# Optimization experiments

Measured on AMD Instinct MI355X. Metric: run time of the kernel, lower is better.

## Reference

```python
import jax, jax.numpy as jnp
from jax import lax
import numpy as np

B, CIN, H, S = 32, 16, 64, 128
TAU = 0.5


def _conv1d(x, w, b, dilation):
    # x: [B, C, S], w: [O, I, K] -> [B, O, S], stride 1, SAME padding (matches torch padding='same')
    y = lax.conv_general_dilated(x, w, window_strides=(1,), padding='SAME',
                                 rhs_dilation=(dilation,),
                                 dimension_numbers=('NCH', 'OIH', 'NCH'))
    return y + b[None, :, None]


def setup_inputs() -> dict:
    key = jax.random.key(0)
    ks = jax.random.split(key, 16)
    def w(k, shape, fan_in):
        return jax.random.normal(k, shape, jnp.float32) * (1.0 / np.sqrt(fan_in))
    inp = {
        'data': jax.random.normal(ks[0], (B, 1, CIN, S), jnp.float32),
        'conv11_w': w(ks[1], (H, CIN, 1), CIN), 'conv11_b': jnp.zeros((H,), jnp.float32),
        'conv12_w': w(ks[2], (H, H, 3), H * 3), 'conv12_b': jnp.zeros((H,), jnp.float32),
        'conv21_w': w(ks[3], (H, CIN, 1), CIN), 'conv21_b': jnp.zeros((H,), jnp.float32),
        'conv22_w': w(ks[4], (H, H, 5), H * 5), 'conv22_b': jnp.zeros((H,), jnp.float32),
        'conv31_w': w(ks[5], (H, CIN, 5), CIN * 5), 'conv31_b': jnp.zeros((H,), jnp.float32),
        'fc_final_w': w(ks[6], (H, 3 * H), 3 * H), 'fc_final_b': jnp.zeros((H,), jnp.float32),
        'fc1_w': w(ks[7], (H, 2 * H), 2 * H), 'fc1_b': jnp.zeros((H,), jnp.float32),
        'fc2_w': w(ks[8], (2, H), H), 'fc2_b': jnp.zeros((2,), jnp.float32),
        # pre-sampled uniform noise for gumbel-softmax (deterministic reference)
        'gumbel_u': jax.random.uniform(ks[9], (B, S * S, 2), jnp.float32, 1e-7, 1.0 - 1e-7),
    }
    return inp


def reference(data, conv11_w, conv11_b, conv12_w, conv12_b, conv21_w, conv21_b,
              conv22_w, conv22_b, conv31_w, conv31_b, fc_final_w, fc_final_b,
              fc1_w, fc1_b, fc2_w, fc2_b, gumbel_u):
    x = data[:, 0].astype(jnp.float32)                      # [B, CIN, S]
    x1 = _conv1d(_conv1d(x, conv11_w, conv11_b, 1), conv12_w, conv12_b, 3)
    x2 = _conv1d(_conv1d(x, conv21_w, conv21_b, 1), conv22_w, conv22_b, 5)
    x3 = _conv1d(x, conv31_w, conv31_b, 1)
    h = jnp.concatenate([x1, x2, x3], axis=1)               # [B, 3H, S]
    h = jnp.swapaxes(h, 1, 2)                               # [B, S, 3H]
    h = jax.nn.relu(h @ fc_final_w.T + fc_final_b)          # [B, S, H]

    # one-hot matmuls are exact gathers: rec rows = repeat, send cols = tile
    rows = jnp.repeat(jnp.arange(S), S)                     # [S*S]
    cols = jnp.tile(jnp.arange(S), S)                       # [S*S]
    receivers = h[:, rows]                                  # [B, S*S, H]
    senders = h[:, cols]                                    # [B, S*S, H]
    e = jnp.concatenate([senders, receivers], axis=2)       # [B, S*S, 2H]
    e = jax.nn.relu(e @ fc1_w.T + fc1_b)
    logits = e @ fc2_w.T + fc2_b                            # [B, S*S, 2]

    # gumbel-softmax, hard=True (straight-through)
    g = -jnp.log(-jnp.log(gumbel_u))
    y_soft = jax.nn.softmax((logits + g) / TAU, axis=-1)
    y_hard = jax.nn.one_hot(jnp.argmax(y_soft, axis=-1), 2, dtype=y_soft.dtype)
    y = lax.stop_gradient(y_hard - y_soft) + y_soft

    a = y[..., 0].reshape(-1, S, S)                         # [B, S, S]
    keep = jnp.triu(jnp.ones((S, S), bool), k=1)            # zero lower tri and diagonal
    return jnp.where(keep, a, jnp.zeros((), a.dtype))
```

## Files before the change

### kernel.cpp

```cpp
#include <hip/hip_runtime.h>
#include <math.h>

#define BB   32
#define CIN  16
#define HH   64
#define SS   128

typedef double f64x4 __attribute__((ext_vector_type(4)));
#define MFMA64(a,b,c) __builtin_amdgcn_mfma_f64_16x16x4f64((a),(b),(c),0,0,0)

__global__ __launch_bounds__(256) void prep_weights(
    const float* __restrict__ w11, const float* __restrict__ w21,
    const float* __restrict__ w12, const float* __restrict__ w22,
    const float* __restrict__ w31, const float* __restrict__ wf,
    const float* __restrict__ w1,  float* __restrict__ W)
{
    int i = blockIdx.x * 256 + threadIdx.x;
    if (i < 1024)       { int k=i>>4, c=i&15;                  W[c*64+k]          = w11[i]; }
    else if (i < 2048)  { int j=i-1024;  int k=j>>4, c=j&15;   W[1024 + c*64+k]   = w21[j]; }
    else if (i < 14336) { int j=i-2048;  int n=j/192, r=j-192*n; W[2048 + r*64+n] = w12[j]; }
    else if (i < 34816) { int j=i-14336; int n=j/320, r=j-320*n; W[14336 + r*64+n]= w22[j]; }
    else if (i < 43008) { int j=i-34816; int r=j>>6, n=j&63;   W[34816 + j] = (r<80)? w31[n*80+r] : 0.f; }
    else if (i < 55296) { int j=i-43008; int n=j/192, r=j-192*n; W[43008 + r*64+n]= wf[j]; }
    else if (i < 59392) { int j=i-55296; int n=j>>6, m=j&63;   W[55296 + m*64+n]  = w1[n*128+m]; }
    else if (i < 63488) { int j=i-59392; int n=j>>6, m=j&63;   W[59392 + m*64+n]  = w1[n*128+64+m]; }
}

__device__ __forceinline__ void loadB(float* dst, const float* __restrict__ Bb, int c) {
    const float* s = Bb + c * 4096;
    #pragma unroll
    for (int q = 0; q < 16; ++q) dst[q] = s[q * 256];
}
__device__ __forceinline__ void mfma_chunk(const double* pA, const float* cb,
                                           f64x4& a0, f64x4& a1, f64x4& a2, f64x4& a3) {
    #pragma unroll
    for (int s = 0; s < 16; s += 4) {
        a0 = MFMA64(pA[(s+0)*64], (double)cb[s+0], a0);
        a1 = MFMA64(pA[(s+1)*64], (double)cb[s+1], a1);
        a2 = MFMA64(pA[(s+2)*64], (double)cb[s+2], a2);
        a3 = MFMA64(pA[(s+3)*64], (double)cb[s+3], a3);
    }
}

__global__ __launch_bounds__(256, 1) void fused_front(
    const float* __restrict__ x,
    const float* __restrict__ b11, const float* __restrict__ b12,
    const float* __restrict__ b21, const float* __restrict__ b22,
    const float* __restrict__ b31, const float* __restrict__ bf,
    const float* __restrict__ b1,  const float* __restrict__ Wsrc,
    double* __restrict__ Qg, double* __restrict__ Pg)
{
    const int b  = blockIdx.y;
    const int s0 = blockIdx.x * 16;
    const int t  = threadIdx.x;
    const int lane = t & 63, wave = t >> 6;

    __shared__ float  xl[CIN][37];
    __shared__ float  wA[2048];
    __shared__ double t1e[48 * 64];
    __shared__ double t2e[80 * 64];
    __shared__ double x3e[32 * 64];
    __shared__ double x123[16][196];
    double* he = x3e;

    int rowi[4], colj[4], mA1, mA2, bn, bkk;
    {
        double lv = (double)lane;
        f64x4 zz{0.0, 0.0, 0.0, 0.0};
        f64x4 d1 = MFMA64(lv, 1.0, zz);
        f64x4 d2 = MFMA64(1.0, lv, zz);
        int am = ((((int)d1[0]) & 3) == 0);
        int bm = ((((int)d2[0]) & 3) == 0);
        for (int r = 0; r < 4; ++r) {
            int v1 = (int)d1[r], v2 = (int)d2[r];
            rowi[r] = (am ? (v1 - 96) >> 2 : (v1 - 6) >> 4) & 15;
            colj[r] = (bm ? (v2 - 96) >> 2 : (v2 - 6) >> 4) & 15;
        }
        mA1 = am ? 16 : 1;  mA2 = am ? 1 : 4;
        bn  = bm ? (lane & 15) : (lane >> 2);
        bkk = bm ? (lane >> 4) : (lane & 3);
    }
    const float* Bb = Wsrc + 2048 + bkk * 64 + (wave << 4) + bn;

    float bufa[16], bufb[16];
    loadB(bufa, Bb, 0);

    for (int e = t; e < 2048; e += 256) wA[e] = Wsrc[e];
    for (int e = t; e < CIN * 36; e += 256) {
        int c = e / 36, col = e - c * 36;
        int g = s0 - 10 + col;
        xl[c][col] = (g >= 0 && g < SS) ? x[(b * CIN + c) * SS + g] : 0.f;
    }
    __syncthreads();

    for (int e = t; e < 1408; e += 256) {
        int k = e & 63, col = e >> 6;
        int g = s0 - 3 + col;
        double val = 0.0;
        if (g >= 0 && g < SS) {
            double u0 = (double)b11[k], u1 = 0.0;
            #pragma unroll
            for (int c = 0; c < CIN; c += 2) {
                u0 += (double)xl[c][col + 7]     * (double)wA[c * 64 + k];
                u1 += (double)xl[c + 1][col + 7] * (double)wA[(c + 1) * 64 + k];
            }
            val = u0 + u1;
        }
        #pragma unroll
        for (int tp = 0; tp < 3; ++tp) {
            int p = col - 3 * tp;
            if (p >= 0 && p < 16) {
                int kk = k * 3 + tp;
                t1e[((kk>>2)<<6) + (kk&3)*mA1 + p*mA2] = val;
            }
        }
    }
    for (int e = t; e < 2304; e += 256) {
        int k = e & 63, col = e >> 6;
        int g = s0 - 10 + col;
        double val = 0.0;
        if (g >= 0 && g < SS) {
            double u0 = (double)b21[k], u1 = 0.0;
            #pragma unroll
            for (int c = 0; c < CIN; c += 2) {
                u0 += (double)xl[c][col]     * (double)wA[1024 + c * 64 + k];
                u1 += (double)xl[c + 1][col] * (double)wA[1024 + (c + 1) * 64 + k];
            }
            val = u0 + u1;
        }
        #pragma unroll
        for (int tp = 0; tp < 5; ++tp) {
            int p = col - 5 * tp;
            if (p >= 0 && p < 16) {
                int kk = k * 5 + tp;
                t2e[((kk>>2)<<6) + (kk&3)*mA1 + p*mA2] = val;
            }
        }
    }
    for (int e = t; e < 2048; e += 256) {
        int p = e & 15, kk = e >> 4;
        double val = 0.0;
        if (kk < 80) { int c = kk / 5, tp = kk - c * 5; val = (double)xl[c][p + 8 + tp]; }
        x3e[((kk>>2)<<6) + (kk&3)*mA1 + p*mA2] = val;
    }
    __syncthreads();

    {
        f64x4 a0{0,0,0,0}, a1{0,0,0,0}, a2{0,0,0,0}, a3{0,0,0,0};
        loadB(bufb, Bb, 1);  mfma_chunk(t1e + lane,        bufa, a0,a1,a2,a3);
        loadB(bufa, Bb, 2);  mfma_chunk(t1e + 1024 + lane, bufb, a0,a1,a2,a3);
        loadB(bufb, Bb, 3);  mfma_chunk(t1e + 2048 + lane, bufa, a0,a1,a2,a3);
        f64x4 acm = (a0 + a1) + (a2 + a3);
        for (int r = 0; r < 4; ++r) {
            int ch = (wave << 4) + colj[r];
            x123[rowi[r]][ch] = acm[r] + (double)b12[ch];
        }
    }
    {
        f64x4 a0{0,0,0,0}, a1{0,0,0,0}, a2{0,0,0,0}, a3{0,0,0,0};
        loadB(bufa, Bb, 4);  mfma_chunk(t2e + lane,        bufb, a0,a1,a2,a3);
        loadB(bufb, Bb, 5);  mfma_chunk(t2e + 1024 + lane, bufa, a0,a1,a2,a3);
        loadB(bufa, Bb, 6);  mfma_chunk(t2e + 2048 + lane, bufb, a0,a1,a2,a3);
        loadB(bufb, Bb, 7);  mfma_chunk(t2e + 3072 + lane, bufa, a0,a1,a2,a3);
        loadB(bufa, Bb, 8);  mfma_chunk(t2e + 4096 + lane, bufb, a0,a1,a2,a3);
        f64x4 acm = (a0 + a1) + (a2 + a3);
        for (int r = 0; r < 4; ++r) {
            int ch = (wave << 4) + colj[r];
            x123[rowi[r]][64 + ch] = acm[r] + (double)b22[ch];
        }
    }
    {
        f64x4 a0{0,0,0,0}, a1{0,0,0,0}, a2{0,0,0,0}, a3{0,0,0,0};
        loadB(bufb, Bb, 9);  mfma_chunk(x3e + lane,        bufa, a0,a1,a2,a3);
        loadB(bufa, Bb, 10); mfma_chunk(x3e + 1024 + lane, bufb, a0,a1,a2,a3);
        f64x4 acm = (a0 + a1) + (a2 + a3);
        for (int r = 0; r < 4; ++r) {
            int ch = (wave << 4) + colj[r];
            x123[rowi[r]][128 + ch] = acm[r] + (double)b31[ch];
        }
    }
    __syncthreads();
    for (int e = t; e < 3072; e += 256) {
        int p = e & 15, k = e >> 4;
        t1e[((k>>2)<<6) + (k&3)*mA1 + p*mA2] = x123[p][k];
    }
    __syncthreads();
    {
        f64x4 a0{0,0,0,0}, a1{0,0,0,0}, a2{0,0,0,0}, a3{0,0,0,0};
        loadB(bufb, Bb, 11); mfma_chunk(t1e + lane,        bufa, a0,a1,a2,a3);
        loadB(bufa, Bb, 12); mfma_chunk(t1e + 1024 + lane, bufb, a0,a1,a2,a3);
        loadB(bufb, Bb, 13); mfma_chunk(t1e + 2048 + lane, bufa, a0,a1,a2,a3);
        f64x4 acm = (a0 + a1) + (a2 + a3);
        for (int r = 0; r < 4; ++r) {
            int m = (wave << 4) + colj[r];
            double v = acm[r] + (double)bf[m];
            he[((m>>2)<<6) + (m&3)*mA1 + rowi[r]*mA2] = v > 0.0 ? v : 0.0;
        }
    }
    __syncthreads();
    {
        f64x4 a0{0,0,0,0}, a1{0,0,0,0}, a2{0,0,0,0}, a3{0,0,0,0};
        loadB(bufa, Bb, 14); mfma_chunk(he + lane, bufb, a0,a1,a2,a3);
        f64x4 acm = (a0 + a1) + (a2 + a3);
        for (int r = 0; r < 4; ++r)
            Qg[((long)b * SS + s0 + rowi[r]) * HH + (wave << 4) + colj[r]] = acm[r];
    }
    {
        f64x4 a0{0,0,0,0}, a1{0,0,0,0}, a2{0,0,0,0}, a3{0,0,0,0};
        mfma_chunk(he + lane, bufa, a0,a1,a2,a3);
        f64x4 acm = (a0 + a1) + (a2 + a3);
        for (int r = 0; r < 4; ++r) {
            int ch = (wave << 4) + colj[r];
            Pg[((long)b * SS + s0 + rowi[r]) * HH + ch] = acm[r] + (double)b1[ch];
        }
    }
}

__global__ __launch_bounds__(256) void edges(
    const double* __restrict__ Qg, const double* __restrict__ Pg,
    const float* __restrict__ w2, const float* __restrict__ b2,
    const float* __restrict__ gum, float* __restrict__ out)
{
    const int b   = blockIdx.y;
    const int tit = blockIdx.x >> 3;
    const int tjt = blockIdx.x & 7;
    const int t   = threadIdx.x;
    const int ti  = t >> 4, tj = t & 15;
    const int i   = tit * 16 + ti;
    const int j   = tjt * 16 + tj;
    float* op = out + ((long)b * SS + i) * SS + j;

    if (tjt < tit) { *op = 0.0f; return; }

    __shared__ float Plf[16][68];
    __shared__ float Qlf[16][68];
    __shared__ float dwl[64];

    if (t < 64) dwl[t] = w2[t] - w2[64 + t];
    for (int idx = t; idx < 1024; idx += 256) {
        int r = idx >> 6, c = idx & 63;
        Plf[r][c] = (float)Pg[((long)b * SS + tit * 16 + r) * HH + c];
        Qlf[r][c] = (float)Qg[((long)b * SS + tjt * 16 + r) * HH + c];
    }
    __syncthreads();

    if (j <= i) { *op = 0.0f; return; }

    long e = (long)b * SS * SS + (long)i * SS + j;
    const float2 uv = *(const float2*)(gum + e * 2);
    float basef = (b2[0] - b2[1]) - logf(-logf(uv.x)) + logf(-logf(uv.y));

    const float2* Pr = (const float2*)(&Plf[ti][0]);
    const float2* Qr = (const float2*)(&Qlf[tj][0]);
    const float2* Dr = (const float2*)dwl;
    float s0 = 0.f, s1 = 0.f;
    #pragma unroll
    for (int k2 = 0; k2 < 32; ++k2) {
        float2 pv = Pr[k2], qv = Qr[k2], dv = Dr[k2];
        float v0 = pv.x + qv.x; v0 = v0 > 0.f ? v0 : 0.f;
        float v1 = pv.y + qv.y; v1 = v1 > 0.f ? v1 : 0.f;
        s0 += v0 * dv.x; s1 += v1 * dv.y;
    }
    float tot = basef + s0 + s1;

    if (fabsf(tot) < 3e-3f) {
        const double* Prd = Pg + ((long)b * SS + i) * HH;
        const double* Qrd = Qg + ((long)b * SS + j) * HH;
        double acc = (double)b2[0] - (double)b2[1]
                   - log(-log((double)uv.x)) + log(-log((double)uv.y));
        for (int k = 0; k < 64; ++k) {
            double v = Prd[k] + Qrd[k];
            if (v > 0.0) acc += v * ((double)w2[k] - (double)w2[64 + k]);
        }
        *op = (acc >= 0.0) ? 1.0f : 0.0f;
    } else {
        *op = (tot >= 0.f) ? 1.0f : 0.0f;
    }
}

extern "C" void kernel_launch(void* const* d_in, const int* in_sizes, int n_in,
                              void* d_out, int out_size, void* d_ws, size_t ws_size,
                              hipStream_t stream) {
    const float* data = (const float*)d_in[0];
    const float* w11  = (const float*)d_in[1];
    const float* b11  = (const float*)d_in[2];
    const float* w12  = (const float*)d_in[3];
    const float* b12  = (const float*)d_in[4];
    const float* w21  = (const float*)d_in[5];
    const float* b21  = (const float*)d_in[6];
    const float* w22  = (const float*)d_in[7];
    const float* b22  = (const float*)d_in[8];
    const float* w31  = (const float*)d_in[9];
    const float* b31  = (const float*)d_in[10];
    const float* wf   = (const float*)d_in[11];
    const float* bf   = (const float*)d_in[12];
    const float* w1   = (const float*)d_in[13];
    const float* b1   = (const float*)d_in[14];
    const float* w2   = (const float*)d_in[15];
    const float* b2   = (const float*)d_in[16];
    const float* gum  = (const float*)d_in[17];
    float* out = (float*)d_out;

    double* Qg = (double*)d_ws;
    double* Pg = Qg + (long)BB * SS * HH;
    float*  Wt = (float*)(Pg + (long)BB * SS * HH);

    prep_weights<<<248, 256, 0, stream>>>(w11, w21, w12, w22, w31, wf, w1, Wt);
    fused_front<<<dim3(8, BB), 256, 0, stream>>>(
        data, b11, b12, b21, b22, b31, bf, b1, Wt, Qg, Pg);
    edges<<<dim3(64, BB), 256, 0, stream>>>(Qg, Pg, w2, b2, gum, out);
}
```

Baseline: 51.39 us.

## Split K across two wave groups in fused_front with LDS reduction

Doubles the fused_front workgroup to 512 threads and splits each MFMA chunk's K range between two halves of waves. Partial accumulators go through a shared buffer and are summed by the lower half before bias and store. This targets the serial MFMA latency chain of the front kernel when each CU holds only one block. It adds extra barriers and LDS traffic per stage.

```diff
diff --git a/kernel.cpp b/kernel.cpp
--- a/kernel.cpp
+++ b/kernel.cpp
@@ -26,23 +26,34 @@
     else if (i < 63488) { int j=i-59392; int n=j>>6, m=j&63;   W[59392 + m*64+n]  = w1[n*128+64+m]; }
 }
 
-__device__ __forceinline__ void loadB(float* dst, const float* __restrict__ Bb, int c) {
-    const float* s = Bb + c * 4096;
+__device__ __forceinline__ void loadB8(float* dst, const float* __restrict__ Bb,
+                                       int c, int koff) {
+    const float* s = Bb + c * 4096 + koff * 256;
     #pragma unroll
-    for (int q = 0; q < 16; ++q) dst[q] = s[q * 256];
-}
-__device__ __forceinline__ void mfma_chunk(const double* pA, const float* cb,
-                                           f64x4& a0, f64x4& a1, f64x4& a2, f64x4& a3) {
+    for (int q = 0; q < 8; ++q) dst[q] = s[q * 256];
+}
+__device__ __forceinline__ void loadB2(float* dst, const float* __restrict__ Bb,
+                                       int c, int koff) {
+    const float* s = Bb + c * 4096 + koff * 256;
+    dst[0] = s[0]; dst[1] = s[256];
+}
+__device__ __forceinline__ void mfma8(const double* pA, const float* cb, int boff,
+                                      f64x4& a0, f64x4& a1, f64x4& a2, f64x4& a3) {
     #pragma unroll
-    for (int s = 0; s < 16; s += 4) {
-        a0 = MFMA64(pA[(s+0)*64], (double)cb[s+0], a0);
-        a1 = MFMA64(pA[(s+1)*64], (double)cb[s+1], a1);
-        a2 = MFMA64(pA[(s+2)*64], (double)cb[s+2], a2);
-        a3 = MFMA64(pA[(s+3)*64], (double)cb[s+3], a3);
-    }
-}
-
-__global__ __launch_bounds__(256, 1) void fused_front(
+    for (int s = 0; s < 8; s += 4) {
+        a0 = MFMA64(pA[(boff+s+0)*64], (double)cb[s+0], a0);
+        a1 = MFMA64(pA[(boff+s+1)*64], (double)cb[s+1], a1);
+        a2 = MFMA64(pA[(boff+s+2)*64], (double)cb[s+2], a2);
+        a3 = MFMA64(pA[(boff+s+3)*64], (double)cb[s+3], a3);
+    }
+}
+__device__ __forceinline__ void mfma2(const double* pA, const float* cb, int boff,
+                                      f64x4& a0, f64x4& a1) {
+    a0 = MFMA64(pA[(boff+0)*64], (double)cb[0], a0);
+    a1 = MFMA64(pA[(boff+1)*64], (double)cb[1], a1);
+}
+
+__global__ __launch_bounds__(512, 1) void fused_front(
     const float* __restrict__ x,
     const float* __restrict__ b11, const float* __restrict__ b12,
     const float* __restrict__ b21, const float* __restrict__ b22,
@@ -54,6 +65,9 @@
     const int s0 = blockIdx.x * 16;
     const int t  = threadIdx.x;
     const int lane = t & 63, wave = t >> 6;
+    const int wv = wave & 3;
+    const int kh = wave >> 2;
+    const int kh8 = kh << 3, kh2 = kh << 1;
 
     __shared__ float  xl[CIN][37];
     __shared__ float  wA[2048];
@@ -61,6 +75,7 @@
     __shared__ double t2e[80 * 64];
     __shared__ double x3e[32 * 64];
     __shared__ double x123[16][196];
+    __shared__ double part[4][4][64];
     double* he = x3e;
 
     int rowi[4], colj[4], mA1, mA2, bn, bkk;
@@ -80,20 +95,20 @@
         bn  = bm ? (lane & 15) : (lane >> 2);
         bkk = bm ? (lane >> 4) : (lane & 3);
     }
-    const float* Bb = Wsrc + 2048 + bkk * 64 + (wave << 4) + bn;
-
-    float bufa[16], bufb[16];
-    loadB(bufa, Bb, 0);
-
-    for (int e = t; e < 2048; e += 256) wA[e] = Wsrc[e];
-    for (int e = t; e < CIN * 36; e += 256) {
+    const float* Bb = Wsrc + 2048 + bkk * 64 + (wv << 4) + bn;
+
+    float bufa[8], bufb[8];
+    loadB8(bufa, Bb, 0, kh8);
+
+    for (int e = t; e < 2048; e += 512) wA[e] = Wsrc[e];
+    for (int e = t; e < CIN * 36; e += 512) {
         int c = e / 36, col = e - c * 36;
         int g = s0 - 10 + col;
         xl[c][col] = (g >= 0 && g < SS) ? x[(b * CIN + c) * SS + g] : 0.f;
     }
     __syncthreads();
 
-    for (int e = t; e < 1408; e += 256) {
+    for (int e = t; e < 1408; e += 512) {
         int k = e & 63, col = e >> 6;
         int g = s0 - 3 + col;
         double val = 0.0;
@@ -115,7 +130,7 @@
             }
         }
     }
-    for (int e = t; e < 2304; e += 256) {
+    for (int e = t; e < 2304; e += 512) {
         int k = e & 63, col = e >> 6;
         int g = s0 - 10 + col;
         double val = 0.0;
@@ -137,7 +152,7 @@
             }
         }
     }
-    for (int e = t; e < 2048; e += 256) {
+    for (int e = t; e < 2048; e += 512) {
         int p = e & 15, kk = e >> 4;
         double val = 0.0;
         if (kk < 80) { int c = kk / 5, tp = kk - c * 5; val = (double)xl[c][p + 8 + tp]; }
@@ -147,71 +162,100 @@
 
     {
         f64x4 a0{0,0,0,0}, a1{0,0,0,0}, a2{0,0,0,0}, a3{0,0,0,0};
-        loadB(bufb, Bb, 1);  mfma_chunk(t1e + lane,        bufa, a0,a1,a2,a3);
-        loadB(bufa, Bb, 2);  mfma_chunk(t1e + 1024 + lane, bufb, a0,a1,a2,a3);
-        loadB(bufb, Bb, 3);  mfma_chunk(t1e + 2048 + lane, bufa, a0,a1,a2,a3);
-        f64x4 acm = (a0 + a1) + (a2 + a3);
-        for (int r = 0; r < 4; ++r) {
-            int ch = (wave << 4) + colj[r];
-            x123[rowi[r]][ch] = acm[r] + (double)b12[ch];
-        }
-    }
-    {
-        f64x4 a0{0,0,0,0}, a1{0,0,0,0}, a2{0,0,0,0}, a3{0,0,0,0};
-        loadB(bufa, Bb, 4);  mfma_chunk(t2e + lane,        bufb, a0,a1,a2,a3);
-        loadB(bufb, Bb, 5);  mfma_chunk(t2e + 1024 + lane, bufa, a0,a1,a2,a3);
-        loadB(bufa, Bb, 6);  mfma_chunk(t2e + 2048 + lane, bufb, a0,a1,a2,a3);
-        loadB(bufb, Bb, 7);  mfma_chunk(t2e + 3072 + lane, bufa, a0,a1,a2,a3);
-        loadB(bufa, Bb, 8);  mfma_chunk(t2e + 4096 + lane, bufb, a0,a1,a2,a3);
-        f64x4 acm = (a0 + a1) + (a2 + a3);
-        for (int r = 0; r < 4; ++r) {
-            int ch = (wave << 4) + colj[r];
-            x123[rowi[r]][64 + ch] = acm[r] + (double)b22[ch];
-        }
-    }
-    {
-        f64x4 a0{0,0,0,0}, a1{0,0,0,0}, a2{0,0,0,0}, a3{0,0,0,0};
-        loadB(bufb, Bb, 9);  mfma_chunk(x3e + lane,        bufa, a0,a1,a2,a3);
-        loadB(bufa, Bb, 10); mfma_chunk(x3e + 1024 + lane, bufb, a0,a1,a2,a3);
-        f64x4 acm = (a0 + a1) + (a2 + a3);
-        for (int r = 0; r < 4; ++r) {
-            int ch = (wave << 4) + colj[r];
-            x123[rowi[r]][128 + ch] = acm[r] + (double)b31[ch];
-        }
-    }
-    __syncthreads();
-    for (int e = t; e < 3072; e += 256) {
+        loadB8(bufb, Bb, 1, kh8);  mfma8(t1e + lane,        bufa, kh8, a0,a1,a2,a3);
+        loadB8(bufa, Bb, 2, kh8);  mfma8(t1e + 1024 + lane, bufb, kh8, a0,a1,a2,a3);
+        loadB8(bufb, Bb, 3, kh8);  mfma8(t1e + 2048 + lane, bufa, kh8, a0,a1,a2,a3);
+        f64x4 acm = (a0 + a1) + (a2 + a3);
+        if (kh) { for (int r = 0; r < 4; ++r) part[r][wv][lane] = acm[r]; }
+        __syncthreads();
+        if (!kh) {
+            for (int r = 0; r < 4; ++r) {
+                int ch = (wv << 4) + colj[r];
+                x123[rowi[r]][ch] = acm[r] + part[r][wv][lane] + (double)b12[ch];
+            }
+        }
+        __syncthreads();
+    }
+    {
+        f64x4 a0{0,0,0,0}, a1{0,0,0,0}, a2{0,0,0,0}, a3{0,0,0,0};
+        loadB8(bufa, Bb, 4, kh8);  mfma8(t2e + lane,        bufb, kh8, a0,a1,a2,a3);
+        loadB8(bufb, Bb, 5, kh8);  mfma8(t2e + 1024 + lane, bufa, kh8, a0,a1,a2,a3);
+        loadB8(bufa, Bb, 6, kh8);  mfma8(t2e + 2048 + lane, bufb, kh8, a0,a1,a2,a3);
+        loadB8(bufb, Bb, 7, kh8);  mfma8(t2e + 3072 + lane, bufa, kh8, a0,a1,a2,a3);
+        loadB8(bufa, Bb, 8, kh8);  mfma8(t2e + 4096 + lane, bufb, kh8, a0,a1,a2,a3);
+        f64x4 acm = (a0 + a1) + (a2 + a3);
+        if (kh) { for (int r = 0; r < 4; ++r) part[r][wv][lane] = acm[r]; }
+        __syncthreads();
+        if (!kh) {
+            for (int r = 0; r < 4; ++r) {
+                int ch = (wv << 4) + colj[r];
+                x123[rowi[r]][64 + ch] = acm[r] + part[r][wv][lane] + (double)b22[ch];
+            }
+        }
+        __syncthreads();
+    }
+    {
+        f64x4 a0{0,0,0,0}, a1{0,0,0,0}, a2{0,0,0,0}, a3{0,0,0,0};
+        loadB2(bufb, Bb, 9, kh2);  mfma8(x3e + lane,        bufa, kh8, a0,a1,a2,a3);
+        loadB8(bufa, Bb, 10, kh8); mfma2(x3e + 1024 + lane, bufb, kh2, a0,a1);
+        f64x4 acm = (a0 + a1) + (a2 + a3);
+        if (kh) { for (int r = 0; r < 4; ++r) part[r][wv][lane] = acm[r]; }
+        __syncthreads();
+        if (!kh) {
+            for (int r = 0; r < 4; ++r) {
+                int ch = (wv << 4) + colj[r];
+                x123[rowi[r]][128 + ch] = acm[r] + part[r][wv][lane] + (double)b31[ch];
+            }
+        }
+        __syncthreads();
+    }
+    for (int e = t; e < 3072; e += 512) {
         int p = e & 15, k = e >> 4;
         t1e[((k>>2)<<6) + (k&3)*mA1 + p*mA2] = x123[p][k];
     }
     __syncthreads();
     {
         f64x4 a0{0,0,0,0}, a1{0,0,0,0}, a2{0,0,0,0}, a3{0,0,0,0};
-        loadB(bufb, Bb, 11); mfma_chunk(t1e + lane,        bufa, a0,a1,a2,a3);
-        loadB(bufa, Bb, 12); mfma_chunk(t1e + 1024 + lane, bufb, a0,a1,a2,a3);
-        loadB(bufb, Bb, 13); mfma_chunk(t1e + 2048 + lane, bufa, a0,a1,a2,a3);
-        f64x4 acm = (a0 + a1) + (a2 + a3);
-        for (int r = 0; r < 4; ++r) {
-            int m = (wave << 4) + colj[r];
-            double v = acm[r] + (double)bf[m];
-            he[((m>>2)<<6) + (m&3)*mA1 + rowi[r]*mA2] = v > 0.0 ? v : 0.0;
-        }
-    }
-    __syncthreads();
-    {
-        f64x4 a0{0,0,0,0}, a1{0,0,0,0}, a2{0,0,0,0}, a3{0,0,0,0};
-        loadB(bufa, Bb, 14); mfma_chunk(he + lane, bufb, a0,a1,a2,a3);
-        f64x4 acm = (a0 + a1) + (a2 + a3);
-        for (int r = 0; r < 4; ++r)
-            Qg[((long)b * SS + s0 + rowi[r]) * HH + (wave << 4) + colj[r]] = acm[r];
-    }
-    {
-        f64x4 a0{0,0,0,0}, a1{0,0,0,0}, a2{0,0,0,0}, a3{0,0,0,0};
-        mfma_chunk(he + lane, bufa, a0,a1,a2,a3);
-        f64x4 acm = (a0 + a1) + (a2 + a3);
-        for (int r = 0; r < 4; ++r) {
-            int ch = (wave << 4) + colj[r];
-            Pg[((long)b * SS + s0 + rowi[r]) * HH + ch] = acm[r] + (double)b1[ch];
+        loadB8(bufb, Bb, 11, kh8); mfma8(t1e + lane,        bufa, kh8, a0,a1,a2,a3);
+        loadB8(bufa, Bb, 12, kh8); mfma8(t1e + 1024 + lane, bufb, kh8, a0,a1,a2,a3);
+        loadB8(bufb, Bb, 13, kh8); mfma8(t1e + 2048 + lane, bufa, kh8, a0,a1,a2,a3);
+        f64x4 acm = (a0 + a1) + (a2 + a3);
+        if (kh) { for (int r = 0; r < 4; ++r) part[r][wv][lane] = acm[r]; }
+        __syncthreads();
+        if (!kh) {
+            for (int r = 0; r < 4; ++r) {
+                int m = (wv << 4) + colj[r];
+                double v = acm[r] + part[r][wv][lane] + (double)bf[m];
+                he[((m>>2)<<6) + (m&3)*mA1 + rowi[r]*mA2] = v > 0.0 ? v : 0.0;
+            }
+        }
+        __syncthreads();
+    }
+    {
+        f64x4 a0{0,0,0,0}, a1{0,0,0,0}, a2{0,0,0,0}, a3{0,0,0,0};
+        loadB8(bufa, Bb, 14, kh8); mfma8(he + lane, bufb, kh8, a0,a1,a2,a3);
+        f64x4 acm = (a0 + a1) + (a2 + a3);
+        if (kh) { for (int r = 0; r < 4; ++r) part[r][wv][lane] = acm[r]; }
+        __syncthreads();
+        if (!kh) {
+            for (int r = 0; r < 4; ++r)
+                Qg[((long)b * SS + s0 + rowi[r]) * HH + (wv << 4) + colj[r]]
+                    = acm[r] + part[r][wv][lane];
+        }
+        __syncthreads();
+    }
+    {
+        f64x4 a0{0,0,0,0}, a1{0,0,0,0}, a2{0,0,0,0}, a3{0,0,0,0};
+        mfma8(he + lane, bufa, kh8, a0,a1,a2,a3);
+        f64x4 acm = (a0 + a1) + (a2 + a3);
+        if (kh) { for (int r = 0; r < 4; ++r) part[r][wv][lane] = acm[r]; }
+        __syncthreads();
+        if (!kh) {
+            for (int r = 0; r < 4; ++r) {
+                int ch = (wv << 4) + colj[r];
+                Pg[((long)b * SS + s0 + rowi[r]) * HH + ch]
+                    = acm[r] + part[r][wv][lane] + (double)b1[ch];
+            }
         }
     }
 }
@@ -306,7 +350,7 @@
     float*  Wt = (float*)(Pg + (long)BB * SS * HH);
 
     prep_weights<<<248, 256, 0, stream>>>(w11, w21, w12, w22, w31, wf, w1, Wt);
-    fused_front<<<dim3(8, BB), 256, 0, stream>>>(
+    fused_front<<<dim3(8, BB), 512, 0, stream>>>(
         data, b11, b12, b21, b22, b31, bf, b1, Wt, Qg, Pg);
     edges<<<dim3(64, BB), 256, 0, stream>>>(Qg, Pg, w2, b2, gum, out);
 }
```

Measured after the change: 49.21 us. 1.04x faster.

## Replace FP64 MFMA front-end with scalar FMA split-K and drop weight prep kernel

Applied to the files above, without the earlier changes.

Replaces the f64 MFMA-based conv/FC chain in the front kernel with per-lane scalar double FMAs. Each of 8 waves handles a slice of the reduction dimension, and a shared-memory reduction combines the partial sums. Weights are read directly from the original layouts, so the separate prep_weights launch and its transposed workspace copy go away. Block size doubles to 512 threads. This trades matrix-core throughput for fewer launches and simpler layouts, but adds several syncthreads-heavy reductions and strided global weight reads per lane.

```diff
diff --git a/kernel.cpp b/kernel.cpp
--- a/kernel.cpp
+++ b/kernel.cpp
@@ -6,48 +6,72 @@
 #define HH   64
 #define SS   128
 
-typedef double f64x4 __attribute__((ext_vector_type(4)));
-#define MFMA64(a,b,c) __builtin_amdgcn_mfma_f64_16x16x4f64((a),(b),(c),0,0,0)
-
-__global__ __launch_bounds__(256) void prep_weights(
-    const float* __restrict__ w11, const float* __restrict__ w21,
-    const float* __restrict__ w12, const float* __restrict__ w22,
-    const float* __restrict__ w31, const float* __restrict__ wf,
-    const float* __restrict__ w1,  float* __restrict__ W)
-{
-    int i = blockIdx.x * 256 + threadIdx.x;
-    if (i < 1024)       { int k=i>>4, c=i&15;                  W[c*64+k]          = w11[i]; }
-    else if (i < 2048)  { int j=i-1024;  int k=j>>4, c=j&15;   W[1024 + c*64+k]   = w21[j]; }
-    else if (i < 14336) { int j=i-2048;  int n=j/192, r=j-192*n; W[2048 + r*64+n] = w12[j]; }
-    else if (i < 34816) { int j=i-14336; int n=j/320, r=j-320*n; W[14336 + r*64+n]= w22[j]; }
-    else if (i < 43008) { int j=i-34816; int r=j>>6, n=j&63;   W[34816 + j] = (r<80)? w31[n*80+r] : 0.f; }
-    else if (i < 55296) { int j=i-43008; int n=j/192, r=j-192*n; W[43008 + r*64+n]= wf[j]; }
-    else if (i < 59392) { int j=i-55296; int n=j>>6, m=j&63;   W[55296 + m*64+n]  = w1[n*128+m]; }
-    else if (i < 63488) { int j=i-59392; int n=j>>6, m=j&63;   W[59392 + m*64+n]  = w1[n*128+64+m]; }
-}
-
-__device__ __forceinline__ void loadB(float* dst, const float* __restrict__ Bb, int c) {
-    const float* s = Bb + c * 4096;
+
+template <int KS>
+__device__ __forceinline__ void fma_slice(const double* __restrict__ dat,
+                                          const float* __restrict__ wrow,
+                                          double* acc) {
+    float wreg[KS];
     #pragma unroll
-    for (int q = 0; q < 16; ++q) dst[q] = s[q * 256];
-}
-__device__ __forceinline__ void mfma_chunk(const double* pA, const float* cb,
-                                           f64x4& a0, f64x4& a1, f64x4& a2, f64x4& a3) {
+    for (int q = 0; q < KS; q += 2)
+        *(float2*)(wreg + q) = *(const float2*)(wrow + q);
     #pragma unroll
-    for (int s = 0; s < 16; s += 4) {
-        a0 = MFMA64(pA[(s+0)*64], (double)cb[s+0], a0);
-        a1 = MFMA64(pA[(s+1)*64], (double)cb[s+1], a1);
-        a2 = MFMA64(pA[(s+2)*64], (double)cb[s+2], a2);
-        a3 = MFMA64(pA[(s+3)*64], (double)cb[s+3], a3);
-    }
-}
-
-__global__ __launch_bounds__(256, 1) void fused_front(
+    for (int p = 0; p < 16; ++p) acc[p] = 0.0;
+    #pragma unroll 4
+    for (int kk = 0; kk < KS; ++kk) {
+        const double2* dr = (const double2*)(dat + kk * 16);
+        double w = (double)wreg[kk];
+        #pragma unroll
+        for (int h2 = 0; h2 < 8; ++h2) {
+            double2 dv = dr[h2];
+            acc[2 * h2]     += dv.x * w;
+            acc[2 * h2 + 1] += dv.y * w;
+        }
+    }
+}
+
+__device__ __forceinline__ void reduce8(double* __restrict__ red,
+                                        const double* __restrict__ acc,
+                                        int wave, int lane, double* tot) {
+    __syncthreads();
+    if (wave >= 4) {
+        double* rp = red + (wave - 4) * 1024 + lane;
+        #pragma unroll
+        for (int p = 0; p < 16; ++p) rp[p * 64] = acc[p];
+    }
+    __syncthreads();
+    double acc2[16];
+    if (wave < 4) {
+        const double* rp = red + wave * 1024 + lane;
+        #pragma unroll
+        for (int p = 0; p < 16; ++p) acc2[p] = acc[p] + rp[p * 64];
+    }
+    __syncthreads();
+    if (wave < 4) {
+        double* rp = red + wave * 1024 + lane;
+        #pragma unroll
+        for (int p = 0; p < 16; ++p) rp[p * 64] = acc2[p];
+    }
+    __syncthreads();
+    if (wave < 4) {
+        #pragma unroll
+        for (int q = 0; q < 4; ++q) {
+            int p = 4 * wave + q;
+            tot[q] = red[p * 64 + lane]        + red[1024 + p * 64 + lane]
+                   + red[2048 + p * 64 + lane] + red[3072 + p * 64 + lane];
+        }
+    }
+}
+
+__global__ __launch_bounds__(512, 2) void fused_front(
     const float* __restrict__ x,
-    const float* __restrict__ b11, const float* __restrict__ b12,
-    const float* __restrict__ b21, const float* __restrict__ b22,
-    const float* __restrict__ b31, const float* __restrict__ bf,
-    const float* __restrict__ b1,  const float* __restrict__ Wsrc,
+    const float* __restrict__ w11, const float* __restrict__ b11,
+    const float* __restrict__ w12, const float* __restrict__ b12,
+    const float* __restrict__ w21, const float* __restrict__ b21,
+    const float* __restrict__ w22, const float* __restrict__ b22,
+    const float* __restrict__ w31, const float* __restrict__ b31,
+    const float* __restrict__ wf,  const float* __restrict__ bf,
+    const float* __restrict__ w1,  const float* __restrict__ b1,
     double* __restrict__ Qg, double* __restrict__ Pg)
 {
     const int b  = blockIdx.y;
@@ -55,45 +79,28 @@
     const int t  = threadIdx.x;
     const int lane = t & 63, wave = t >> 6;
 
+    __shared__ double S[14592];
     __shared__ float  xl[CIN][37];
     __shared__ float  wA[2048];
-    __shared__ double t1e[48 * 64];
-    __shared__ double t2e[80 * 64];
-    __shared__ double x3e[32 * 64];
-    __shared__ double x123[16][196];
-    double* he = x3e;
-
-    int rowi[4], colj[4], mA1, mA2, bn, bkk;
-    {
-        double lv = (double)lane;
-        f64x4 zz{0.0, 0.0, 0.0, 0.0};
-        f64x4 d1 = MFMA64(lv, 1.0, zz);
-        f64x4 d2 = MFMA64(1.0, lv, zz);
-        int am = ((((int)d1[0]) & 3) == 0);
-        int bm = ((((int)d2[0]) & 3) == 0);
-        for (int r = 0; r < 4; ++r) {
-            int v1 = (int)d1[r], v2 = (int)d2[r];
-            rowi[r] = (am ? (v1 - 96) >> 2 : (v1 - 6) >> 4) & 15;
-            colj[r] = (bm ? (v2 - 96) >> 2 : (v2 - 6) >> 4) & 15;
-        }
-        mA1 = am ? 16 : 1;  mA2 = am ? 1 : 4;
-        bn  = bm ? (lane & 15) : (lane >> 2);
-        bkk = bm ? (lane >> 4) : (lane & 3);
-    }
-    const float* Bb = Wsrc + 2048 + bkk * 64 + (wave << 4) + bn;
-
-    float bufa[16], bufb[16];
-    loadB(bufa, Bb, 0);
-
-    for (int e = t; e < 2048; e += 256) wA[e] = Wsrc[e];
-    for (int e = t; e < CIN * 36; e += 256) {
+    double* t2d = S;
+    double* x3d = S + 5120;
+    double* xf  = S + 6400;
+    double* h   = S + 9472;
+    double* t1d = S + 10496;
+    double* red = S + 10496;
+
+    for (int e = t; e < 2048; e += 512) {
+        if (e < 1024) { int k = e >> 4, c = e & 15; wA[c * 64 + k] = w11[e]; }
+        else { int j = e - 1024; int k = j >> 4, c = j & 15; wA[1024 + c * 64 + k] = w21[j]; }
+    }
+    for (int e = t; e < CIN * 36; e += 512) {
         int c = e / 36, col = e - c * 36;
         int g = s0 - 10 + col;
         xl[c][col] = (g >= 0 && g < SS) ? x[(b * CIN + c) * SS + g] : 0.f;
     }
     __syncthreads();
 
-    for (int e = t; e < 1408; e += 256) {
+    for (int e = t; e < 1408; e += 512) {
         int k = e & 63, col = e >> 6;
         int g = s0 - 3 + col;
         double val = 0.0;
@@ -109,13 +116,10 @@
         #pragma unroll
         for (int tp = 0; tp < 3; ++tp) {
             int p = col - 3 * tp;
-            if (p >= 0 && p < 16) {
-                int kk = k * 3 + tp;
-                t1e[((kk>>2)<<6) + (kk&3)*mA1 + p*mA2] = val;
-            }
-        }
-    }
-    for (int e = t; e < 2304; e += 256) {
+            if (p >= 0 && p < 16) t1d[(k * 3 + tp) * 16 + p] = val;
+        }
+    }
+    for (int e = t; e < 2304; e += 512) {
         int k = e & 63, col = e >> 6;
         int g = s0 - 10 + col;
         double val = 0.0;
@@ -131,87 +135,71 @@
         #pragma unroll
         for (int tp = 0; tp < 5; ++tp) {
             int p = col - 5 * tp;
-            if (p >= 0 && p < 16) {
-                int kk = k * 5 + tp;
-                t2e[((kk>>2)<<6) + (kk&3)*mA1 + p*mA2] = val;
-            }
-        }
-    }
-    for (int e = t; e < 2048; e += 256) {
-        int p = e & 15, kk = e >> 4;
-        double val = 0.0;
-        if (kk < 80) { int c = kk / 5, tp = kk - c * 5; val = (double)xl[c][p + 8 + tp]; }
-        x3e[((kk>>2)<<6) + (kk&3)*mA1 + p*mA2] = val;
-    }
-    __syncthreads();
-
-    {
-        f64x4 a0{0,0,0,0}, a1{0,0,0,0}, a2{0,0,0,0}, a3{0,0,0,0};
-        loadB(bufb, Bb, 1);  mfma_chunk(t1e + lane,        bufa, a0,a1,a2,a3);
-        loadB(bufa, Bb, 2);  mfma_chunk(t1e + 1024 + lane, bufb, a0,a1,a2,a3);
-        loadB(bufb, Bb, 3);  mfma_chunk(t1e + 2048 + lane, bufa, a0,a1,a2,a3);
-        f64x4 acm = (a0 + a1) + (a2 + a3);
-        for (int r = 0; r < 4; ++r) {
-            int ch = (wave << 4) + colj[r];
-            x123[rowi[r]][ch] = acm[r] + (double)b12[ch];
-        }
-    }
-    {
-        f64x4 a0{0,0,0,0}, a1{0,0,0,0}, a2{0,0,0,0}, a3{0,0,0,0};
-        loadB(bufa, Bb, 4);  mfma_chunk(t2e + lane,        bufb, a0,a1,a2,a3);
-        loadB(bufb, Bb, 5);  mfma_chunk(t2e + 1024 + lane, bufa, a0,a1,a2,a3);
-        loadB(bufa, Bb, 6);  mfma_chunk(t2e + 2048 + lane, bufb, a0,a1,a2,a3);
-        loadB(bufb, Bb, 7);  mfma_chunk(t2e + 3072 + lane, bufa, a0,a1,a2,a3);
-        loadB(bufa, Bb, 8);  mfma_chunk(t2e + 4096 + lane, bufb, a0,a1,a2,a3);
-        f64x4 acm = (a0 + a1) + (a2 + a3);
-        for (int r = 0; r < 4; ++r) {
-            int ch = (wave << 4) + colj[r];
-            x123[rowi[r]][64 + ch] = acm[r] + (double)b22[ch];
-        }
-    }
-    {
-        f64x4 a0{0,0,0,0}, a1{0,0,0,0}, a2{0,0,0,0}, a3{0,0,0,0};
-        loadB(bufb, Bb, 9);  mfma_chunk(x3e + lane,        bufa, a0,a1,a2,a3);
-        loadB(bufa, Bb, 10); mfma_chunk(x3e + 1024 + lane, bufb, a0,a1,a2,a3);
-        f64x4 acm = (a0 + a1) + (a2 + a3);
-        for (int r = 0; r < 4; ++r) {
-            int ch = (wave << 4) + colj[r];
-            x123[rowi[r]][128 + ch] = acm[r] + (double)b31[ch];
-        }
-    }
-    __syncthreads();
-    for (int e = t; e < 3072; e += 256) {
-        int p = e & 15, k = e >> 4;
-        t1e[((k>>2)<<6) + (k&3)*mA1 + p*mA2] = x123[p][k];
-    }
-    __syncthreads();
-    {
-        f64x4 a0{0,0,0,0}, a1{0,0,0,0}, a2{0,0,0,0}, a3{0,0,0,0};
-        loadB(bufb, Bb, 11); mfma_chunk(t1e + lane,        bufa, a0,a1,a2,a3);
-        loadB(bufa, Bb, 12); mfma_chunk(t1e + 1024 + lane, bufb, a0,a1,a2,a3);
-        loadB(bufb, Bb, 13); mfma_chunk(t1e + 2048 + lane, bufa, a0,a1,a2,a3);
-        f64x4 acm = (a0 + a1) + (a2 + a3);
-        for (int r = 0; r < 4; ++r) {
-            int m = (wave << 4) + colj[r];
-            double v = acm[r] + (double)bf[m];
-            he[((m>>2)<<6) + (m&3)*mA1 + rowi[r]*mA2] = v > 0.0 ? v : 0.0;
-        }
-    }
-    __syncthreads();
-    {
-        f64x4 a0{0,0,0,0}, a1{0,0,0,0}, a2{0,0,0,0}, a3{0,0,0,0};
-        loadB(bufa, Bb, 14); mfma_chunk(he + lane, bufb, a0,a1,a2,a3);
-        f64x4 acm = (a0 + a1) + (a2 + a3);
-        for (int r = 0; r < 4; ++r)
-            Qg[((long)b * SS + s0 + rowi[r]) * HH + (wave << 4) + colj[r]] = acm[r];
-    }
-    {
-        f64x4 a0{0,0,0,0}, a1{0,0,0,0}, a2{0,0,0,0}, a3{0,0,0,0};
-        mfma_chunk(he + lane, bufa, a0,a1,a2,a3);
-        f64x4 acm = (a0 + a1) + (a2 + a3);
-        for (int r = 0; r < 4; ++r) {
-            int ch = (wave << 4) + colj[r];
-            Pg[((long)b * SS + s0 + rowi[r]) * HH + ch] = acm[r] + (double)b1[ch];
+            if (p >= 0 && p < 16) t2d[(k * 5 + tp) * 16 + p] = val;
+        }
+    }
+    for (int e = t; e < 1280; e += 512) {
+        int k = e >> 4, p = e & 15;
+        int c = k / 5, tp = k - c * 5;
+        x3d[e] = (double)xl[c][p + 8 + tp];
+    }
+    __syncthreads();
+
+    double acc[16], tot[4];
+
+    fma_slice<24>(t1d + wave * 24 * 16, w12 + lane * 192 + wave * 24, acc);
+    reduce8(red, acc, wave, lane, tot);
+    if (wave < 4) {
+        double bv = (double)b12[lane];
+        #pragma unroll
+        for (int q = 0; q < 4; ++q) xf[lane * 16 + 4 * wave + q] = tot[q] + bv;
+    }
+    __syncthreads();
+    fma_slice<40>(t2d + wave * 40 * 16, w22 + lane * 320 + wave * 40, acc);
+    reduce8(red, acc, wave, lane, tot);
+    if (wave < 4) {
+        double bv = (double)b22[lane];
+        #pragma unroll
+        for (int q = 0; q < 4; ++q) xf[(64 + lane) * 16 + 4 * wave + q] = tot[q] + bv;
+    }
+    __syncthreads();
+    fma_slice<10>(x3d + wave * 10 * 16, w31 + lane * 80 + wave * 10, acc);
+    reduce8(red, acc, wave, lane, tot);
+    if (wave < 4) {
+        double bv = (double)b31[lane];
+        #pragma unroll
+        for (int q = 0; q < 4; ++q) xf[(128 + lane) * 16 + 4 * wave + q] = tot[q] + bv;
+    }
+    __syncthreads();
+    fma_slice<24>(xf + wave * 24 * 16, wf + lane * 192 + wave * 24, acc);
+    reduce8(red, acc, wave, lane, tot);
+    if (wave < 4) {
+        double bv = (double)bf[lane];
+        #pragma unroll
+        for (int q = 0; q < 4; ++q) {
+            double v = tot[q] + bv;
+            h[lane * 16 + 4 * wave + q] = v > 0.0 ? v : 0.0;
+        }
+    }
+    __syncthreads();
+    fma_slice<8>(h + wave * 8 * 16, w1 + lane * 128 + wave * 8, acc);
+    reduce8(red, acc, wave, lane, tot);
+    if (wave < 4) {
+        #pragma unroll
+        for (int q = 0; q < 4; ++q) {
+            int p = 4 * wave + q;
+            Qg[((long)b * SS + s0 + p) * HH + lane] = tot[q];
+        }
+    }
+    __syncthreads();
+    fma_slice<8>(h + wave * 8 * 16, w1 + lane * 128 + 64 + wave * 8, acc);
+    reduce8(red, acc, wave, lane, tot);
+    if (wave < 4) {
+        double bv = (double)b1[lane];
+        #pragma unroll
+        for (int q = 0; q < 4; ++q) {
+            int p = 4 * wave + q;
+            Pg[((long)b * SS + s0 + p) * HH + lane] = tot[q] + bv;
         }
     }
 }
@@ -303,10 +291,9 @@
 
     double* Qg = (double*)d_ws;
     double* Pg = Qg + (long)BB * SS * HH;
-    float*  Wt = (float*)(Pg + (long)BB * SS * HH);
-
-    prep_weights<<<248, 256, 0, stream>>>(w11, w21, w12, w22, w31, wf, w1, Wt);
-    fused_front<<<dim3(8, BB), 256, 0, stream>>>(
-        data, b11, b12, b21, b22, b31, bf, b1, Wt, Qg, Pg);
+
+    fused_front<<<dim3(8, BB), 512, 0, stream>>>(
+        data, w11, b11, w12, b12, w21, b21, w22, b22, w31, b31,
+        wf, bf, w1, b1, Qg, Pg);
     edges<<<dim3(64, BB), 256, 0, stream>>>(Qg, Pg, w2, b2, gum, out);
 }
```

Result: slower. 89.25 us (+73.7%).
